# Kernel tuning notes

Hardware: AMD Instinct MI355X
Metric: run time of the kernel (lower is better)

## Reference

```python
import jax, jax.numpy as jnp
from jax import lax
import numpy as np

IMG_H, IMG_W = 800.0, 1344.0
NMS_PRE, NMS_POST, MAX_NUM = 2000, 1000, 1000
IOU_THR = 0.7
STRIDES = [4, 8, 16, 32, 64]
SIZES = [(200, 336), (100, 168), (50, 84), (25, 42), (13, 21)]
MAX_RATIO = float(abs(np.log(16.0 / 1000.0)))  # mmdet wh_ratio_clip


def _make_anchors(H, W, stride):
    # mmdet AnchorGenerator: scales=[8], ratios=[0.5,1,2], base_size=stride
    ratios = np.array([0.5, 1.0, 2.0])
    scale = 8.0
    hr = np.sqrt(ratios)
    wr = 1.0 / hr
    ws = stride * wr * scale
    hs = stride * hr * scale
    c = stride / 2.0
    base = np.stack([c - 0.5 * ws, c - 0.5 * hs, c + 0.5 * ws, c + 0.5 * hs], 1)  # [3,4]
    xx, yy = np.meshgrid(np.arange(W) * stride, np.arange(H) * stride)
    shifts = np.stack([xx, yy, xx, yy], -1).reshape(-1, 1, 4)  # [H*W,1,4]
    return (shifts + base[None]).reshape(-1, 4).astype(np.float32)  # order (H,W,A)


def setup_inputs() -> dict:
    key = jax.random.key(0)
    inp = {}
    for i, (H, W) in enumerate(SIZES):
        k1, k2, key = jax.random.split(key, 3)
        inp[f"cls{i}"] = jax.random.normal(k1, (2, 3, H, W), jnp.float32)
        inp[f"bbox{i}"] = jax.random.normal(k2, (2, 12, H, W), jnp.float32) * 0.5
        inp[f"anc{i}"] = jnp.asarray(_make_anchors(H, W, STRIDES[i]))
    return inp


def _delta2bbox(deltas, anchors):
    # deltas, anchors: [..., 4]; means=0, stds=1
    dx, dy = deltas[..., 0], deltas[..., 1]
    dw = jnp.clip(deltas[..., 2], -MAX_RATIO, MAX_RATIO)
    dh = jnp.clip(deltas[..., 3], -MAX_RATIO, MAX_RATIO)
    pw = anchors[..., 2] - anchors[..., 0]
    ph = anchors[..., 3] - anchors[..., 1]
    px = (anchors[..., 0] + anchors[..., 2]) * 0.5
    py = (anchors[..., 1] + anchors[..., 3]) * 0.5
    gw = pw * jnp.exp(dw)
    gh = ph * jnp.exp(dh)
    gx = px + pw * dx
    gy = py + ph * dy
    x1 = jnp.clip(gx - 0.5 * gw, 0.0, IMG_W)
    y1 = jnp.clip(gy - 0.5 * gh, 0.0, IMG_H)
    x2 = jnp.clip(gx + 0.5 * gw, 0.0, IMG_W)
    y2 = jnp.clip(gy + 0.5 * gh, 0.0, IMG_H)
    return jnp.stack([x1, y1, x2, y2], axis=-1)


def _pairwise_iou(b):
    # b: [N,4]
    area = (b[:, 2] - b[:, 0]) * (b[:, 3] - b[:, 1])
    lt = jnp.maximum(b[:, None, :2], b[None, :, :2])
    rb = jnp.minimum(b[:, None, 2:], b[None, :, 2:])
    wh = jnp.clip(rb - lt, 0.0, None)
    inter = wh[..., 0] * wh[..., 1]
    union = area[:, None] + area[None, :] - inter
    return inter / jnp.maximum(union, 1e-6)


def _nms_single(boxes, scores):
    # boxes [NMS_PRE,4], scores [NMS_PRE] (one image). Greedy NMS, keep NMS_POST.
    N = scores.shape[0]
    order = jnp.argsort(-scores)
    b = boxes[order]
    s = scores[order]
    iou = _pairwise_iou(lax.stop_gradient(b))
    idx = jnp.arange(N)

    def step(supp, i):
        keep_i = jnp.logical_not(supp[i])
        supp = supp | (keep_i & (iou[i] > IOU_THR) & (idx > i))
        return supp, keep_i

    _, keeps = lax.scan(step, jnp.zeros((N,), bool), idx)
    s_kept = jnp.where(keeps, s, -1.0)
    top_s, top_i = lax.top_k(s_kept, NMS_POST)
    return b[top_i], top_s


def _process_level(cls, bbox, anchors):
    B = cls.shape[0]
    # [B,A,H,W] -> [B,H,W,A] -> [B,N]; [B,A*4,H,W] -> [B,H,W,A*4] -> [B,N,4]
    scores = jax.nn.sigmoid(cls.transpose(0, 2, 3, 1).reshape(B, -1))
    deltas = bbox.transpose(0, 2, 3, 1).reshape(B, -1, 4)
    N = scores.shape[1]
    if N < NMS_PRE:  # pad small levels to min_num_bboxes (nms_pre)
        pad = NMS_PRE - N
        scores = jnp.pad(scores, ((0, 0), (0, pad)), constant_values=-1.0)
        deltas = jnp.pad(deltas, ((0, 0), (0, pad), (0, 0)))
        anchors = jnp.pad(anchors, ((0, pad), (0, 0)))
        top_s = scores
        top_i = jnp.broadcast_to(jnp.arange(NMS_PRE), (B, NMS_PRE))
    else:
        top_s, top_i = lax.top_k(scores, NMS_PRE)
    deltas_g = jnp.take_along_axis(deltas, top_i[..., None], axis=1)  # [B,NMS_PRE,4]
    anc_g = anchors[top_i]  # [B,NMS_PRE,4]
    props = _delta2bbox(deltas_g, anc_g)
    boxes, sc = jax.vmap(_nms_single)(props, top_s)
    return sc, boxes


def _forward(cls_list, bbox_list, anc_list):
    mlvl_scores, mlvl_props = [], []
    for cls, bbox, anc in zip(cls_list, bbox_list, anc_list):
        s, p = _process_level(cls, bbox, anc)
        mlvl_scores.append(s)
        mlvl_props.append(p)
    scores = jnp.concatenate(mlvl_scores, axis=1)      # [B, 5*NMS_POST]
    proposals = jnp.concatenate(mlvl_props, axis=1)    # [B, 5*NMS_POST, 4]
    _, topk_inds = lax.top_k(scores, MAX_NUM)
    return jnp.take_along_axis(proposals, topk_inds[..., None], axis=1)  # [B, MAX_NUM, 4]


def reference(cls0, cls1, cls2, cls3, cls4,
              bbox0, bbox1, bbox2, bbox3, bbox4,
              anc0, anc1, anc2, anc3, anc4):
    return _forward([cls0, cls1, cls2, cls3, cls4],
                    [bbox0, bbox1, bbox2, bbox3, bbox4],
                    [anc0, anc1, anc2, anc3, anc4])
```

## Files before the change

### kernel.cpp

```cpp
#include <hip/hip_runtime.h>
#include <cmath>


#define NPRE 2000
#define NPOST 1000

static __device__ __forceinline__ unsigned int flipf_dev(float f) {
  unsigned int u = __float_as_uint(f);
  return (u & 0x80000000u) ? ~u : (u | 0x80000000u);
}
static __device__ __forceinline__ float unflipf_dev(unsigned int k) {
  unsigned int u = (k & 0x80000000u) ? (k ^ 0x80000000u) : ~k;
  return __uint_as_float(u);
}
static __device__ __forceinline__ unsigned long long flip64_dev(double d) {
  unsigned long long u = (unsigned long long)__double_as_longlong(d);
  return (u & 0x8000000000000000ull) ? ~u : (u | 0x8000000000000000ull);
}

struct RPNParams {
  const float* cls[5];
  const float* bbox[5];
  const float* anc[5];
  unsigned int* hist;
  unsigned int* mainCount;
  unsigned int* candCount;
  unsigned int* Bstar;
  unsigned long long* mainEK;
  unsigned long long* candEK;
  unsigned long long* ekG;
  unsigned int* partialR;
  double* selBoxes;
  double* selScores;
  unsigned long long* mask;
  double* postScores;
  float* postBoxes;
  unsigned int* partial;
  float* out;
};

__device__ __constant__ int c_NL[5]  = {201600, 50400, 12600, 3150, 819};
__device__ __constant__ int c_HW[5]  = {67200, 16800, 4200, 1050, 273};
__device__ __constant__ int c_BPT[8] = {99, 99, 25, 25, 7, 7, 2, 2};
__device__ __constant__ int c_BPT12[8] = {25, 25, 7, 7, 2, 2, 1, 1};

static __device__ __forceinline__ void map_block(int bx, int& t, int& chunk) {
  int start = 0;
  t = 0;
  for (int k = 0; k < 8; k++) {
    if (bx < start + c_BPT[k]) { t = k; break; }
    start += c_BPT[k];
  }
  chunk = bx - start;
}
static __device__ __forceinline__ void map_block12(int bx, int& t, int& chunk) {
  int start = 0;
  t = 0;
  for (int k = 0; k < 8; k++) {
    if (bx < start + c_BPT12[k]) { t = k; break; }
    start += c_BPT12[k];
  }
  chunk = bx - start;
}

__global__ __launch_bounds__(1024) void k_hist(RPNParams p) {
  __shared__ unsigned int lh[4096];
  int t, chunk;
  map_block12(blockIdx.x, t, chunk);
  int l = t >> 1, b = t & 1;
  int N = c_NL[l], HW = c_HW[l];
  const float* cls = p.cls[l] + (size_t)b * 3 * HW;
  int tid = threadIdx.x;
  for (int i = tid; i < 4096; i += 1024) lh[i] = 0;
  __syncthreads();
  int base = chunk * 8192 + tid;
#pragma unroll
  for (int k = 0; k < 8; k++) {
    int n = base + k * 1024;
    if (n < N) {
      int a = n % 3, hw = n / 3;
      unsigned int key = flipf_dev(cls[a * HW + hw]);
      atomicAdd(&lh[key >> 20], 1u);
    }
  }
  __syncthreads();
  unsigned int* hout = p.hist + (size_t)blockIdx.x * 4096;
  for (int i = tid; i < 4096; i += 1024) hout[i] = lh[i];
}

__global__ void k_find(RPNParams p) {
  int t = blockIdx.x;
  __shared__ unsigned int H[4096];
  __shared__ unsigned int S[1024];
  __shared__ int gsel;
  __shared__ unsigned int baseAbove;
  int tid = threadIdx.x;
  int start = 0;
  for (int k = 0; k < t; k++) start += c_BPT12[k];
  int bpt = c_BPT12[t];
  for (int bin = tid; bin < 4096; bin += 1024) {
    unsigned int s = 0;
    for (int bb = 0; bb < bpt; bb++)
      s += p.hist[(size_t)(start + bb) * 4096 + bin];
    H[bin] = s;
  }
  __syncthreads();
  S[tid] = H[tid * 4] + H[tid * 4 + 1] + H[tid * 4 + 2] + H[tid * 4 + 3];
  __syncthreads();
  for (int off = 1; off < 1024; off <<= 1) {
    unsigned int add = (tid + off < 1024) ? S[tid + off] : 0u;
    __syncthreads();
    S[tid] += add;
    __syncthreads();
  }
  const unsigned int need = NPRE;
  if (S[tid] >= need && (tid == 1023 || S[tid + 1] < need)) {
    gsel = tid;
    baseAbove = (tid == 1023) ? 0u : S[tid + 1];
  }
  __syncthreads();
  if (tid == 0) {
    int gg = gsel;
    unsigned int c = baseAbove;
    int bstar = gg * 4;
    for (int bb = 3; bb >= 0; bb--) {
      c += H[gg * 4 + bb];
      if (c >= need) { bstar = gg * 4 + bb; break; }
    }
    p.Bstar[t] = (unsigned int)bstar;
  }
}

__global__ void k_compact(RPNParams p) {
  int t, chunk;
  map_block(blockIdx.x, t, chunk);
  int l = t >> 1, b = t & 1;
  int N = c_NL[l], HW = c_HW[l];
  const float* cls = p.cls[l] + (size_t)b * 3 * HW;
  unsigned int Bs = p.Bstar[t];
  int base = chunk * 2048 + threadIdx.x;
  for (int k = 0; k < 2; k++) {
    int n = base + k * 1024;
    if (n < N) {
      int a = n % 3, hw = n / 3;
      unsigned int key = flipf_dev(cls[a * HW + hw]);
      unsigned int hi = key >> 20;
      unsigned long long ek =
          ((unsigned long long)key << 32) | (unsigned int)(~(unsigned int)n);
      if (hi > Bs) {
        unsigned int pos = atomicAdd(&p.mainCount[t], 1u);
        if (pos < 2048u) p.mainEK[(size_t)t * 2048 + pos] = ek;
      } else if (hi == Bs) {
        unsigned int pos = atomicAdd(&p.candCount[t], 1u);
        if (pos < 8192u) p.candEK[(size_t)t * 8192 + pos] = ek;
      }
    }
  }
}

__global__ void k_fill(RPNParams p) {
  int t = blockIdx.x;
  int l = t >> 1, b = t & 1;
  int N = c_NL[l], HW = c_HW[l];
  int tid = threadIdx.x;
  unsigned long long* ekG = p.ekG + (size_t)t * 2048;
  if (N >= NPRE) {
    unsigned int cGT = min(p.mainCount[t], 2000u);
    unsigned int nC = min(p.candCount[t], 8192u);
    unsigned int needIn = 2000u - cGT;
    for (unsigned int m = tid; m < cGT; m += 256)
      ekG[m] = p.mainEK[(size_t)t * 2048 + m];
    const unsigned long long* cek = p.candEK + (size_t)t * 8192;
    __shared__ unsigned long long sl[256];
    for (unsigned int estrip = 0; estrip < nC; estrip += 2048) {
      unsigned long long ve[8];
      unsigned int r[8];
      bool en[8];
#pragma unroll
      for (int k = 0; k < 8; k++) {
        unsigned int e = estrip + k * 256 + tid;
        en[k] = e < nC;
        ve[k] = en[k] ? cek[e] : 0ull;
        r[k] = 0;
      }
      for (unsigned int jb = 0; jb < nC; jb += 256) {
        __syncthreads();
        sl[tid] = (jb + tid < nC) ? cek[jb + tid] : 0ull;
        __syncthreads();
        int lim = (int)min(256u, nC - jb);
        for (int j = 0; j < lim; j++) {
          unsigned long long vj = sl[j];
#pragma unroll
          for (int k = 0; k < 8; k++) r[k] += (vj > ve[k]) ? 1u : 0u;
        }
      }
#pragma unroll
      for (int k = 0; k < 8; k++)
        if (en[k] && r[k] < needIn) ekG[cGT + r[k]] = ve[k];
    }
    for (unsigned int r2 = 2000u + tid; r2 < 2048u; r2 += 256)
      ekG[r2] = (unsigned long long)(unsigned int)(~r2);
  } else {
    const float* cls = p.cls[l] + (size_t)b * 3 * HW;
    for (int r = tid; r < 2048; r += 256) {
      if (r < N) {
        int a = r % 3, hw = r / 3;
        unsigned int key = flipf_dev(cls[a * HW + hw]);
        ekG[r] = ((unsigned long long)key << 32) |
                 (unsigned int)(~(unsigned int)r);
      } else {
        ekG[r] = (unsigned long long)(unsigned int)(~(unsigned int)r);
      }
    }
  }
}

__global__ void k_rank(RPNParams p) {
  int t = blockIdx.x >> 3;
  int s = blockIdx.x & 7;
  int tid = threadIdx.x;
  __shared__ unsigned long long sl[256];
  const unsigned long long* ekG = p.ekG + (size_t)t * 2048;
  sl[tid] = ekG[s * 256 + tid];
  __syncthreads();
  unsigned long long ve[8];
  unsigned int r[8];
#pragma unroll
  for (int k = 0; k < 8; k++) {
    ve[k] = ekG[k * 256 + tid];
    r[k] = 0;
  }
  for (int j = 0; j < 256; j++) {
    unsigned long long vj = sl[j];
#pragma unroll
    for (int k = 0; k < 8; k++) r[k] += (vj > ve[k]) ? 1u : 0u;
  }
  unsigned int* out = p.partialR + ((size_t)t * 8 + s) * 2048;
#pragma unroll
  for (int k = 0; k < 8; k++) out[k * 256 + tid] = r[k];
}

__global__ void k_scatter(RPNParams p) {
  int t = blockIdx.x;
  int l = t >> 1, b = t & 1;
  int HW = c_HW[l];
  int tid = threadIdx.x;
  __shared__ unsigned long long srt[2048];
  const unsigned long long* ekG = p.ekG + (size_t)t * 2048;
  for (int e = tid; e < 2048; e += 1024) {
    unsigned int rk = 0;
#pragma unroll
    for (int s = 0; s < 8; s++)
      rk += p.partialR[((size_t)t * 8 + s) * 2048 + e];
    srt[rk] = ekG[e];
  }
  __syncthreads();

  const double RCLIP = fabs(log(16.0 / 1000.0));
  const float* bbx = p.bbox[l] + (size_t)b * 12 * HW;
  const float* anc = p.anc[l];
  for (int r = tid; r < NPRE; r += 1024) {
    unsigned long long v = srt[r];
    unsigned int key = (unsigned int)(v >> 32);
    double* SB = p.selBoxes + ((size_t)t * NPRE + r) * 4;
    if (key == 0u) {
      SB[0] = 0.0; SB[1] = 0.0; SB[2] = 0.0; SB[3] = 0.0;
      p.selScores[(size_t)t * NPRE + r] = -1.0;
    } else {
      unsigned int idx = ~(unsigned int)(v & 0xFFFFFFFFull);
      int a = (int)(idx % 3u);
      int hw = (int)(idx / 3u);
      double d0 = (double)bbx[(a * 4 + 0) * HW + hw];
      double d1 = (double)bbx[(a * 4 + 1) * HW + hw];
      double d2 = (double)bbx[(a * 4 + 2) * HW + hw];
      double d3 = (double)bbx[(a * 4 + 3) * HW + hw];
      double a0 = (double)anc[(size_t)idx * 4 + 0];
      double a1 = (double)anc[(size_t)idx * 4 + 1];
      double a2 = (double)anc[(size_t)idx * 4 + 2];
      double a3 = (double)anc[(size_t)idx * 4 + 3];
      double dw = fmin(fmax(d2, -RCLIP), RCLIP);
      double dh = fmin(fmax(d3, -RCLIP), RCLIP);
      double pw = a2 - a0, ph = a3 - a1;
      double px = (a0 + a2) * 0.5, py = (a1 + a3) * 0.5;
      double gw = pw * exp(dw), gh = ph * exp(dh);
      double gx = px + pw * d0, gy = py + ph * d1;
      double x1 = fmin(fmax(gx - 0.5 * gw, 0.0), 1344.0);
      double y1 = fmin(fmax(gy - 0.5 * gh, 0.0), 800.0);
      double x2 = fmin(fmax(gx + 0.5 * gw, 0.0), 1344.0);
      double y2 = fmin(fmax(gy + 0.5 * gh, 0.0), 800.0);
      SB[0] = x1; SB[1] = y1; SB[2] = x2; SB[3] = y2;
      float f = unflipf_dev(key);
      p.selScores[(size_t)t * NPRE + r] = 1.0 / (1.0 + exp(-(double)f));
    }
  }
}

__global__ __launch_bounds__(640) void k_iou(RPNParams p) {
  int bx = blockIdx.x;
  int t = bx / 25;
  int q = bx % 25;
  __shared__ float X1[2048], Y1[2048], X2[2048], Y2[2048], AR[2048];
  const double* SB = p.selBoxes + (size_t)t * NPRE * 4;
  for (int i = threadIdx.x; i < 2048; i += 640) {
    float x1 = 0.f, y1 = 0.f, x2 = 0.f, y2 = 0.f;
    if (i < NPRE) {
      x1 = (float)SB[i * 4 + 0]; y1 = (float)SB[i * 4 + 1];
      x2 = (float)SB[i * 4 + 2]; y2 = (float)SB[i * 4 + 3];
    }
    X1[i] = x1; Y1[i] = y1; X2[i] = x2; Y2[i] = y2;
    AR[i] = (x2 - x1) * (y2 - y1);
  }
  __syncthreads();
  int wave = threadIdx.x >> 6, lane = threadIdx.x & 63;
  int g = q + 25 * wave;
  int i0 = g * 8;
  float x1i[8], y1i[8], x2i[8], y2i[8], ai[8];
#pragma unroll
  for (int r = 0; r < 8; r++) {
    int i = i0 + r;
    x1i[r] = X1[i]; y1i[r] = Y1[i]; x2i[r] = X2[i]; y2i[r] = Y2[i];
    ai[r] = AR[i];
  }
  int c0 = i0 >> 6;
  int j0 = c0 * 64 + lane;
  float cx1 = X1[j0], cy1 = Y1[j0], cx2 = X2[j0], cy2 = Y2[j0], car = AR[j0];
  for (int k = c0; k < 32; k++) {
    float nx1 = 0.f, ny1 = 0.f, nx2 = 0.f, ny2 = 0.f, nar = 0.f;
    if (k + 1 < 32) {
      int jn = (k + 1) * 64 + lane;
      nx1 = X1[jn]; ny1 = Y1[jn]; nx2 = X2[jn]; ny2 = Y2[jn];
      nar = AR[jn];
    }
    int j = k * 64 + lane;
    bool jin = j < NPRE;
    bool pred[8], need[8];
    bool needAny = false;
#pragma unroll
    for (int r = 0; r < 8; r++) {
      int i = i0 + r;
      bool valid = jin && (j > i);
      float lx = fmaxf(x1i[r], cx1), ly = fmaxf(y1i[r], cy1);
      float rx = fminf(x2i[r], cx2), ry = fminf(y2i[r], cy2);
      float w = fmaxf(rx - lx, 0.0f), h = fmaxf(ry - ly, 0.0f);
      float inter = w * h;
      float uni = fmaxf(ai[r] + car - inter, 1e-6f);
      float diff = inter - 0.7f * uni;
      pred[r] = valid && (diff > 0.0f);
      need[r] = valid && (fabsf(diff) <= 4.0f + 1e-5f * uni);
      needAny |= need[r];
    }
    if (__any(needAny)) {
#pragma unroll
      for (int r = 0; r < 8; r++) {
        if (need[r]) {
          int i = i0 + r;
          double a0 = SB[i * 4 + 0], b0 = SB[i * 4 + 1];
          double a2 = SB[i * 4 + 2], b2 = SB[i * 4 + 3];
          double c0d = SB[j * 4 + 0], d0 = SB[j * 4 + 1];
          double c2 = SB[j * 4 + 2], d2 = SB[j * 4 + 3];
          double dai = (a2 - a0) * (b2 - b0);
          double daj = (c2 - c0d) * (d2 - d0);
          double lxd = fmax(a0, c0d), lyd = fmax(b0, d0);
          double rxd = fmin(a2, c2), ryd = fmin(b2, d2);
          double wd = fmax(rxd - lxd, 0.0), hd = fmax(ryd - lyd, 0.0);
          double interd = wd * hd;
          double unid = fmax(dai + daj - interd, 1e-6);
          pred[r] = (interd / unid) > 0.7;
        }
      }
    }
#pragma unroll
    for (int r = 0; r < 8; r++) {
      unsigned long long word = __ballot(pred[r]);
      if (lane == 0) p.mask[((size_t)t * NPRE + i0 + r) * 32 + k] = word;
    }
    cx1 = nx1; cy1 = ny1; cx2 = nx2; cy2 = ny2; car = nar;
  }
}

#define GRP_N 63
#define RING 6
__global__ __launch_bounds__(512) void k_greedy(RPNParams p) {
  int t = blockIdx.x;
  int tid = threadIdx.x;
  __shared__ unsigned long long ring[RING * 1024];
  __shared__ int ready[GRP_N];
  __shared__ int cons_s;
  __shared__ unsigned long long kw[32], aw[32], bw[32];
  __shared__ unsigned int prefA[33], prefB[33];
  volatile int* rdy = ready;
  volatile int* cons = &cons_s;
  const unsigned long long* MK = p.mask + (size_t)t * NPRE * 32;
  for (int i = tid; i < GRP_N; i += 512) ready[i] = 0;
  if (tid == 0) cons_s = 0;
  __syncthreads();

  int wave = tid >> 6, lane = tid & 63;
  if (wave >= 1) {
    for (int g = wave - 1; g < GRP_N; g += 7) {
      while (g - *cons >= RING) __builtin_amdgcn_s_sleep(1);
      unsigned long long v[16];
#pragma unroll
      for (int k = 0; k < 16; k++) {
        int idx = k * 64 + lane;
        int row = g * 32 + (idx >> 5);
        v[k] = (row < NPRE) ? MK[(size_t)row * 32 + (idx & 31)] : 0ull;
      }
      int slot = g % RING;
#pragma unroll
      for (int k = 0; k < 16; k++)
        ring[slot * 1024 + k * 64 + lane] = v[k];
      __threadfence_block();
      if (lane == 0) rdy[g] = 1;
    }
  } else {
    unsigned long long supp = 0ull, keep = 0ull;
    for (int g = 0; g < GRP_N; g++) {
      while (rdy[g] == 0) { }
      __threadfence_block();
      int slot = g % RING;
      int c = g >> 1;
      int base = (g & 1) * 32;
      unsigned long long rv[32];
#pragma unroll
      for (int r = 0; r < 32; r++)
        rv[r] = ring[slot * 1024 + r * 32 + (lane & 31)];
      unsigned int sh = (unsigned int)(supp >> base);
      unsigned int s32 = (unsigned int)__builtin_amdgcn_readlane((int)sh, c);
      unsigned int kg = 0;
#pragma unroll
      for (int r = 0; r < 32; r++) {
        unsigned int rvh = (unsigned int)(rv[r] >> base);
        bool kp = (s32 & (1u << r)) == 0u;
        kg |= kp ? (1u << r) : 0u;
        s32 |= kp ? rvh : 0u;
      }
      kg = (unsigned int)__builtin_amdgcn_readlane((int)kg, c);
      unsigned long long acc0 = 0ull, acc1 = 0ull;
#pragma unroll
      for (int r = 0; r < 32; r += 2) {
        acc0 |= ((kg >> r) & 1u) ? rv[r] : 0ull;
        acc1 |= ((kg >> (r + 1)) & 1u) ? rv[r + 1] : 0ull;
      }
      supp |= acc0 | acc1;
      keep |= (lane == c) ? ((unsigned long long)kg << base) : 0ull;
      __threadfence_block();
      if (lane == 63) *cons = g + 1;
    }
    if (lane < 32) kw[lane] = keep;
  }
  __syncthreads();

  for (int ch = wave; ch < 32; ch += 8) {
    int i = ch * 64 + lane;
    bool inr = i < NPRE;
    bool kb = inr && ((kw[ch] >> lane) & 1ull);
    bool A = kb && (inr ? (p.selScores[(size_t)t * NPRE + i] > -0.5) : false);
    bool B = inr && !A;
    unsigned long long wa = __ballot(A);
    unsigned long long wb = __ballot(B);
    if (lane == 0) { aw[ch] = wa; bw[ch] = wb; }
  }
  __syncthreads();
  if (tid == 0) {
    unsigned int ca = 0, cb = 0;
    for (int w = 0; w < 32; w++) {
      prefA[w] = ca; ca += __popcll(aw[w]);
      prefB[w] = cb; cb += __popcll(bw[w]);
    }
    prefA[32] = ca; prefB[32] = cb;
  }
  __syncthreads();
  unsigned int KA = prefA[32];
  for (int i = tid; i < NPRE; i += 512) {
    int w = i >> 6, bpos = i & 63;
    unsigned long long below = (bpos == 0) ? 0ull : (~0ull >> (64 - bpos));
    bool kb = (kw[w] >> bpos) & 1ull;
    double s = p.selScores[(size_t)t * NPRE + i];
    bool A = kb && (s > -0.5);
    unsigned int slot;
    double outs;
    if (A) {
      slot = prefA[w] + (unsigned int)__popcll(aw[w] & below);
      outs = s;
    } else {
      slot = KA + prefB[w] + (unsigned int)__popcll(bw[w] & below);
      outs = -1.0;
    }
    if (slot < NPOST) {
      p.postScores[(size_t)t * NPOST + slot] = outs;
      const double* SB = p.selBoxes + ((size_t)t * NPRE + i) * 4;
      float* PB = p.postBoxes + ((size_t)t * NPOST + slot) * 4;
      PB[0] = (float)SB[0]; PB[1] = (float)SB[1];
      PB[2] = (float)SB[2]; PB[3] = (float)SB[3];
    }
  }
}

__global__ void k_finalA(RPNParams p) {
  int bx = blockIdx.x;
  int b = bx / 80;
  int rem = bx % 80;
  int s = rem >> 2;
  int ec = rem & 3;
  int j0 = s * 256;
  __shared__ unsigned long long kj[256];
  int tid = threadIdx.x;
  {
    int e = j0 + tid;
    unsigned long long v = 0ull;
    if (e < 5000) {
      int l = e / 1000, slot = e - l * 1000;
      int t = l * 2 + b;
      v = flip64_dev(p.postScores[(size_t)t * NPOST + slot]);
    }
    kj[tid] = v;
  }
  __syncthreads();
  int eidx[5];
  unsigned long long ke[5];
  unsigned int r[5];
#pragma unroll
  for (int k = 0; k < 5; k++) {
    int e = ec * 1280 + k * 256 + tid;
    eidx[k] = (e < 5000) ? e : -1;
    if (eidx[k] >= 0) {
      int l = e / 1000, slot = e - l * 1000;
      int t = l * 2 + b;
      ke[k] = flip64_dev(p.postScores[(size_t)t * NPOST + slot]);
    } else {
      ke[k] = 0ull;
    }
    r[k] = 0;
  }
  for (int j = 0; j < 256; j++) {
    unsigned long long vj = kj[j];
    int jg = j0 + j;
#pragma unroll
    for (int k = 0; k < 5; k++)
      r[k] += (vj > ke[k] || (vj == ke[k] && jg < eidx[k])) ? 1u : 0u;
  }
#pragma unroll
  for (int k = 0; k < 5; k++)
    if (eidx[k] >= 0)
      p.partial[((size_t)b * 20 + s) * 5000 + eidx[k]] = r[k];
}

__global__ void k_finalB(RPNParams p) {
  int b = blockIdx.x / 5;
  int ch = blockIdx.x % 5;
  int tid = threadIdx.x;
  if (tid < 1000) {
    int e = ch * 1000 + tid;
    unsigned int r = 0;
#pragma unroll
    for (int s = 0; s < 20; s++)
      r += p.partial[((size_t)b * 20 + s) * 5000 + e];
    if (r < NPOST) {
      int l = e / 1000, slot = e - l * 1000;
      int t = l * 2 + b;
      const float* PB = p.postBoxes + ((size_t)t * NPOST + slot) * 4;
      float* O = p.out + ((size_t)b * NPOST + r) * 4;
      O[0] = PB[0]; O[1] = PB[1]; O[2] = PB[2]; O[3] = PB[3];
    }
  }
}

extern "C" void kernel_launch(void* const* d_in, const int* in_sizes, int n_in,
                              void* d_out, int out_size, void* d_ws,
                              size_t ws_size, hipStream_t stream) {
  RPNParams p;
  bool interleaved = (n_in >= 2) && (in_sizes[1] == 4 * in_sizes[0]);
  for (int l = 0; l < 5; l++) {
    if (interleaved) {
      p.cls[l]  = (const float*)d_in[3 * l + 0];
      p.bbox[l] = (const float*)d_in[3 * l + 1];
      p.anc[l]  = (const float*)d_in[3 * l + 2];
    } else {
      p.cls[l]  = (const float*)d_in[l];
      p.bbox[l] = (const float*)d_in[5 + l];
      p.anc[l]  = (const float*)d_in[10 + l];
    }
  }
  char* w = (char*)d_ws;
  size_t off = 0;
  auto alloc = [&](size_t bytes) {
    off = (off + 255) & ~(size_t)255;
    void* r = w + off;
    off += bytes;
    return r;
  };
  p.mainCount = (unsigned int*)alloc(10 * 4);
  p.candCount = (unsigned int*)alloc(10 * 4);
  size_t zbytes = off;
  p.hist       = (unsigned int*)alloc((size_t)70 * 4096 * 4);
  p.Bstar      = (unsigned int*)alloc(10 * 4);
  p.mainEK     = (unsigned long long*)alloc((size_t)10 * 2048 * 8);
  p.candEK     = (unsigned long long*)alloc((size_t)10 * 8192 * 8);
  p.ekG        = (unsigned long long*)alloc((size_t)10 * 2048 * 8);
  p.partialR   = (unsigned int*)alloc((size_t)10 * 8 * 2048 * 4);
  p.selBoxes   = (double*)alloc((size_t)10 * NPRE * 4 * 8);
  p.selScores  = (double*)alloc((size_t)10 * NPRE * 8);
  p.mask       = (unsigned long long*)alloc((size_t)10 * NPRE * 32 * 8);
  p.postScores = (double*)alloc((size_t)10 * NPOST * 8);
  p.postBoxes  = (float*)alloc((size_t)10 * NPOST * 4 * 4);
  p.partial    = (unsigned int*)alloc((size_t)2 * 20 * 5000 * 4);
  p.out = (float*)d_out;
  (void)ws_size; (void)out_size;

  hipMemsetAsync(d_ws, 0, zbytes, stream);
  k_hist<<<dim3(70), dim3(1024), 0, stream>>>(p);
  k_find<<<dim3(8), dim3(1024), 0, stream>>>(p);
  k_compact<<<dim3(266), dim3(1024), 0, stream>>>(p);
  k_fill<<<dim3(10), dim3(256), 0, stream>>>(p);
  k_rank<<<dim3(80), dim3(256), 0, stream>>>(p);
  k_scatter<<<dim3(10), dim3(1024), 0, stream>>>(p);
  k_iou<<<dim3(250), dim3(640), 0, stream>>>(p);
  k_greedy<<<dim3(10), dim3(512), 0, stream>>>(p);
  k_finalA<<<dim3(160), dim3(256), 0, stream>>>(p);
  k_finalB<<<dim3(10), dim3(1024), 0, stream>>>(p);
}
```

Baseline: 467.3 us.

## Refine radix-select histogram to 14 bits and simplify candidate ranking

Widens the top-k histogram from 4096 to 16384 bins (key >> 18), so the threshold bin holds far fewer candidates and the quadratic rank pass in k_fill has much less work. The shared-memory tiled rank loop is replaced by a plain per-thread loop over global candidates, which the smaller candidate count is meant to make affordable. In exchange, the histogram uses 64KB of LDS per block, writes and reads four times more global histogram data, and k_find sums 16 bins per thread.

```diff
diff --git a/kernel.cpp b/kernel.cpp
--- a/kernel.cpp
+++ b/kernel.cpp
@@ -64,14 +64,14 @@
 }
 
 __global__ __launch_bounds__(1024) void k_hist(RPNParams p) {
-  __shared__ unsigned int lh[4096];
+  __shared__ unsigned int lh[16384];
   int t, chunk;
   map_block12(blockIdx.x, t, chunk);
   int l = t >> 1, b = t & 1;
   int N = c_NL[l], HW = c_HW[l];
   const float* cls = p.cls[l] + (size_t)b * 3 * HW;
   int tid = threadIdx.x;
-  for (int i = tid; i < 4096; i += 1024) lh[i] = 0;
+  for (int i = tid; i < 16384; i += 1024) lh[i] = 0;
   __syncthreads();
   int base = chunk * 8192 + tid;
 #pragma unroll
@@ -80,17 +80,17 @@
     if (n < N) {
       int a = n % 3, hw = n / 3;
       unsigned int key = flipf_dev(cls[a * HW + hw]);
-      atomicAdd(&lh[key >> 20], 1u);
-    }
-  }
-  __syncthreads();
-  unsigned int* hout = p.hist + (size_t)blockIdx.x * 4096;
-  for (int i = tid; i < 4096; i += 1024) hout[i] = lh[i];
-}
-
-__global__ void k_find(RPNParams p) {
+      atomicAdd(&lh[key >> 18], 1u);
+    }
+  }
+  __syncthreads();
+  unsigned int* hout = p.hist + (size_t)blockIdx.x * 16384;
+  for (int i = tid; i < 16384; i += 1024) hout[i] = lh[i];
+}
+
+__global__ __launch_bounds__(1024) void k_find(RPNParams p) {
   int t = blockIdx.x;
-  __shared__ unsigned int H[4096];
+  __shared__ unsigned int H[16384];
   __shared__ unsigned int S[1024];
   __shared__ int gsel;
   __shared__ unsigned int baseAbove;
@@ -98,14 +98,19 @@
   int start = 0;
   for (int k = 0; k < t; k++) start += c_BPT12[k];
   int bpt = c_BPT12[t];
-  for (int bin = tid; bin < 4096; bin += 1024) {
+  for (int bin = tid; bin < 16384; bin += 1024) {
     unsigned int s = 0;
     for (int bb = 0; bb < bpt; bb++)
-      s += p.hist[(size_t)(start + bb) * 4096 + bin];
+      s += p.hist[(size_t)(start + bb) * 16384 + bin];
     H[bin] = s;
   }
   __syncthreads();
-  S[tid] = H[tid * 4] + H[tid * 4 + 1] + H[tid * 4 + 2] + H[tid * 4 + 3];
+  {
+    unsigned int s = 0;
+#pragma unroll
+    for (int k = 0; k < 16; k++) s += H[tid * 16 + k];
+    S[tid] = s;
+  }
   __syncthreads();
   for (int off = 1; off < 1024; off <<= 1) {
     unsigned int add = (tid + off < 1024) ? S[tid + off] : 0u;
@@ -122,10 +127,10 @@
   if (tid == 0) {
     int gg = gsel;
     unsigned int c = baseAbove;
-    int bstar = gg * 4;
-    for (int bb = 3; bb >= 0; bb--) {
-      c += H[gg * 4 + bb];
-      if (c >= need) { bstar = gg * 4 + bb; break; }
+    int bstar = gg * 16;
+    for (int bb = 15; bb >= 0; bb--) {
+      c += H[gg * 16 + bb];
+      if (c >= need) { bstar = gg * 16 + bb; break; }
     }
     p.Bstar[t] = (unsigned int)bstar;
   }
@@ -144,7 +149,7 @@
     if (n < N) {
       int a = n % 3, hw = n / 3;
       unsigned int key = flipf_dev(cls[a * HW + hw]);
-      unsigned int hi = key >> 20;
+      unsigned int hi = key >> 18;
       unsigned long long ek =
           ((unsigned long long)key << 32) | (unsigned int)(~(unsigned int)n);
       if (hi > Bs) {
@@ -171,32 +176,11 @@
     for (unsigned int m = tid; m < cGT; m += 256)
       ekG[m] = p.mainEK[(size_t)t * 2048 + m];
     const unsigned long long* cek = p.candEK + (size_t)t * 8192;
-    __shared__ unsigned long long sl[256];
-    for (unsigned int estrip = 0; estrip < nC; estrip += 2048) {
-      unsigned long long ve[8];
-      unsigned int r[8];
-      bool en[8];
-#pragma unroll
-      for (int k = 0; k < 8; k++) {
-        unsigned int e = estrip + k * 256 + tid;
-        en[k] = e < nC;
-        ve[k] = en[k] ? cek[e] : 0ull;
-        r[k] = 0;
-      }
-      for (unsigned int jb = 0; jb < nC; jb += 256) {
-        __syncthreads();
-        sl[tid] = (jb + tid < nC) ? cek[jb + tid] : 0ull;
-        __syncthreads();
-        int lim = (int)min(256u, nC - jb);
-        for (int j = 0; j < lim; j++) {
-          unsigned long long vj = sl[j];
-#pragma unroll
-          for (int k = 0; k < 8; k++) r[k] += (vj > ve[k]) ? 1u : 0u;
-        }
-      }
-#pragma unroll
-      for (int k = 0; k < 8; k++)
-        if (en[k] && r[k] < needIn) ekG[cGT + r[k]] = ve[k];
+    for (unsigned int e = tid; e < nC; e += 256) {
+      unsigned long long ve = cek[e];
+      unsigned int r = 0;
+      for (unsigned int j = 0; j < nC; j++) r += (cek[j] > ve) ? 1u : 0u;
+      if (r < needIn) ekG[cGT + r] = ve;
     }
     for (unsigned int r2 = 2000u + tid; r2 < 2048u; r2 += 256)
       ekG[r2] = (unsigned long long)(unsigned int)(~r2);
@@ -593,7 +577,7 @@
   p.mainCount = (unsigned int*)alloc(10 * 4);
   p.candCount = (unsigned int*)alloc(10 * 4);
   size_t zbytes = off;
-  p.hist       = (unsigned int*)alloc((size_t)70 * 4096 * 4);
+  p.hist       = (unsigned int*)alloc((size_t)70 * 16384 * 4);
   p.Bstar      = (unsigned int*)alloc(10 * 4);
   p.mainEK     = (unsigned long long*)alloc((size_t)10 * 2048 * 8);
   p.candEK     = (unsigned long long*)alloc((size_t)10 * 8192 * 8);
```

Measured after the change: 448.0 us. -4.1%, faster.
